# Optimization experiments

Hardware: AMD Instinct MI355X
Metric: run time of the kernel (lower is better)

Reference implementation:

```python
import jax, jax.numpy as jnp
import numpy as np

B, T, D, H, L, W = 32, 512, 256, 8, 2, 10
NQ = 10000
HD = D // H


def setup_inputs():
    key = jax.random.key(0)
    ks = jax.random.split(key, 16)
    def n(k, shape, s=0.02):
        return jax.random.normal(k, shape, jnp.float32) * s
    return {
        "q": jax.random.randint(ks[0], (B, T), 0, NQ),
        "s": jax.random.randint(ks[1], (B, T), 0, 2),
        "q_embed": n(ks[2], (NQ + 1, D)),
        "s_embed": n(ks[3], (2, D)),
        "pos_embed": n(ks[4], (512, D)),
        "fusion_w": n(ks[5], (2 * D, D)),
        "fusion_b": jnp.zeros((D,), jnp.float32),
        "in_proj_w": n(ks[6], (L, D, 3 * D)),
        "in_proj_b": jnp.zeros((L, 3 * D), jnp.float32),
        "out_proj_w": n(ks[7], (L, D, D)),
        "out_proj_b": jnp.zeros((L, D), jnp.float32),
        "ln1_g": jnp.ones((L, D), jnp.float32),
        "ln1_b": jnp.zeros((L, D), jnp.float32),
        "ln2_g": jnp.ones((L, D), jnp.float32),
        "ln2_b": jnp.zeros((L, D), jnp.float32),
        "ff1_w": n(ks[8], (L, D, 4 * D)),
        "ff1_b": jnp.zeros((L, 4 * D), jnp.float32),
        "ff2_w": n(ks[9], (L, 4 * D, D)),
        "ff2_b": jnp.zeros((L, D), jnp.float32),
        "sw1": n(ks[10], (6, 32), 0.1),
        "sb1": jnp.zeros((32,), jnp.float32),
        "sw2": n(ks[11], (32, D // 4), 0.1),
        "sb2": jnp.zeros((D // 4,), jnp.float32),
        "cw1": n(ks[12], (D + D // 4, D)),
        "cb1": jnp.zeros((D,), jnp.float32),
        "cw2": n(ks[13], (D, 1)),
        "cb2": jnp.zeros((1,), jnp.float32),
    }


def _ln(x, g, b):
    mu = jnp.mean(x, -1, keepdims=True)
    var = jnp.mean(jnp.square(x - mu), -1, keepdims=True)
    return (x - mu) * jax.lax.rsqrt(var + 1e-5) * g + b


def _sliding_sum(x, w):
    # sum over trailing window of size w ending at each t, via prefix sums
    c = jnp.concatenate([jnp.zeros((x.shape[0], 1), x.dtype), jnp.cumsum(x, axis=1)], axis=1)
    t = jnp.arange(x.shape[1])
    return c[:, t + 1] - c[:, jnp.maximum(t + 1 - w, 0)]


def _stats(s, mask):
    # vectorized version of _extract_statistics (prefix-sum sliding windows)
    mf = mask.astype(jnp.float32)
    sf = s.astype(jnp.float32) * mf
    valid = _sliding_sum(mf, W)
    correct_rate = _sliding_sum(sf, W) / (valid + 1e-6)
    rc = _sliding_sum(mf, 5)
    recent_correct = _sliding_sum(sf, 5) / (rc + 1e-6)
    trans = ((s[:, 1:] != s[:, :-1]) & mask[:, 1:] & mask[:, :-1]).astype(jnp.float32)
    diff = jnp.concatenate([jnp.zeros((s.shape[0], 1), jnp.float32), trans], axis=1)
    change_rate = _sliding_sum(diff, W - 1) / (valid + 1e-6)
    # max consecutive equal run within each trailing window of size W
    sp = jnp.pad(s, ((0, 0), (W - 1, 0)))
    mp = jnp.pad(mask, ((0, 0), (W - 1, 0)))
    win_s = [sp[:, j:j + T] for j in range(W)]
    win_m = [mp[:, j:j + T] for j in range(W)]
    run = win_m[0].astype(jnp.float32)
    mx = run
    for j in range(1, W):  # fixed small window, not a data-dim loop
        eq = (win_s[j] == win_s[j - 1]) & win_m[j - 1]
        run = win_m[j].astype(jnp.float32) * (jnp.where(eq, run, 0.0) + 1.0)
        mx = jnp.maximum(mx, run)
    rel = jnp.broadcast_to(jnp.arange(T, dtype=jnp.float32) / max(T, 100), s.shape)
    cov = valid / W
    return jnp.stack([correct_rate, recent_correct, change_rate, mx / W, rel, cov], axis=-1)


def reference(q, s, q_embed, s_embed, pos_embed, fusion_w, fusion_b, in_proj_w, in_proj_b,
              out_proj_w, out_proj_b, ln1_g, ln1_b, ln2_g, ln2_b, ff1_w, ff1_b, ff2_w, ff2_b,
              sw1, sb1, sw2, sb2, cw1, cb1, cw2, cb2):
    mask = s >= 0
    qm = jnp.where(mask, q, 0)
    sm = jnp.where(mask, s, 0)
    h = jnp.concatenate([q_embed[qm], s_embed[sm]], axis=-1)  # [B,T,2D]
    h = jax.nn.relu(h @ fusion_w + fusion_b) + pos_embed[:T][None]
    causal = jnp.tril(jnp.ones((T, T), bool))
    allowed = causal[None, None] & mask[:, None, None, :]
    scale = 1.0 / (HD ** 0.5)
    for l in range(L):
        qkv = h @ in_proj_w[l] + in_proj_b[l]
        qh, kh, vh = jnp.split(qkv, 3, axis=-1)
        qh = qh.reshape(B, T, H, HD).transpose(0, 2, 1, 3)
        kh = kh.reshape(B, T, H, HD).transpose(0, 2, 1, 3)
        vh = vh.reshape(B, T, H, HD).transpose(0, 2, 1, 3)
        scores = jnp.einsum('bhqd,bhkd->bhqk', qh, kh) * scale
        scores = jnp.where(allowed, scores, -1e9)
        attn = jax.nn.softmax(scores, axis=-1)
        o = jnp.einsum('bhqk,bhkd->bhqd', attn, vh).transpose(0, 2, 1, 3).reshape(B, T, D)
        h = _ln(h + (o @ out_proj_w[l] + out_proj_b[l]), ln1_g[l], ln1_b[l])
        ff = jax.nn.gelu(h @ ff1_w[l] + ff1_b[l], approximate=False) @ ff2_w[l] + ff2_b[l]
        h = _ln(h + ff, ln2_g[l], ln2_b[l])
    sfeat = _stats(sm, mask)  # [B,T,6]
    semb = jax.nn.relu(sfeat @ sw1 + sb1) @ sw2 + sb2  # [B,T,D//4]
    comb = jnp.concatenate([h, semb], axis=-1)
    logits = (jax.nn.relu(comb @ cw1 + cb1) @ cw2 + cb2)[..., 0]
    return jnp.where(mask, logits, -1e9)
```

## Files before the change

### kernel.cpp

```cpp
#include <hip/hip_runtime.h>
#include <hip/hip_bf16.h>
#include <cmath>


using short8 = __attribute__((ext_vector_type(8))) short;
using short4v = __attribute__((ext_vector_type(4))) short;
using f32x4  = __attribute__((ext_vector_type(4))) float;

__device__ inline float gelu_f(float x) {
    return 0.5f * x * (1.0f + erff(x * 0.70710678118654752f));
}

__device__ inline short f2bf(float x) {
    union { float f; unsigned u; } v; v.f = x;
    return (short)((v.u + 0x7fffu + ((v.u >> 16) & 1u)) >> 16);
}

__device__ inline float bf2f(short v) {
    union { unsigned u; float f; } x; x.u = ((unsigned)(unsigned short)v) << 16;
    return x.f;
}

__device__ inline unsigned packbf(float lo, float hi) {
    union { float f; unsigned u; } a, b; a.f = lo; b.f = hi;
    unsigned ra = (a.u + 0x7fffu + ((a.u >> 16) & 1u)) >> 16;
    unsigned rb = (b.u + 0x7fffu + ((b.u >> 16) & 1u)) >> 16;
    return (rb << 16) | (ra & 0xffffu);
}

#define GLOAD16(gp, lp) __builtin_amdgcn_global_load_lds( \
    (const __attribute__((address_space(1))) void*)(gp), \
    (__attribute__((address_space(3))) void*)(lp), 16, 0, 0)

__global__ __launch_bounds__(256) void prep(
    const float* __restrict__ fusion_w, const float* __restrict__ in_proj_w,
    const float* __restrict__ out_proj_w, const float* __restrict__ ff1_w,
    const float* __restrict__ ff2_w, const float* __restrict__ cw1,
    short* __restrict__ wts,
    const int* __restrict__ q, const int* __restrict__ s,
    const float* __restrict__ qe, const float* __restrict__ se,
    short* __restrict__ A,
    short* __restrict__ semb,
    const float* __restrict__ sw1, const float* __restrict__ sb1,
    const float* __restrict__ sw2, const float* __restrict__ sb2)
{
    __shared__ float tile[32][33];
    __shared__ float sv_sh[512];
    __shared__ float m_sh[512];
    __shared__ float sw2_sh[2048];

    if (blockIdx.x < 1744) {
        const int b0[10]      = {0,128,320,512,576,640,896,1152,1408,1664};
        const int Ks[10]      = {512,256,256,256,256,256,256,1024,1024,320};
        const int Ns[10]      = {256,768,768,256,256,1024,1024,256,256,256};
        const int sidx[10]    = {0,1,1,2,2,3,3,4,4,5};
        const size_t soff[10] = {0,0,196608,0,65536,0,262144,0,262144,0};
        const size_t doff[10] = {0,131072,327680,524288,589824,655360,917504,1179648,1441792,1703936};
        const float* srcs[6] = {fusion_w, in_proj_w, out_proj_w, ff1_w, ff2_w, cw1};
        int bid = blockIdx.x;
        int mi = 0;
        while (mi < 9 && bid >= b0[mi + 1]) ++mi;
        int bl = bid - b0[mi];
        int K = Ks[mi], N = Ns[mi];
        int tx = bl % (N >> 5), ty = bl / (N >> 5);
        const float* src = srcs[sidx[mi]] + soff[mi];
        short* dst = wts + doff[mi];
        int c = threadIdx.x & 31, r = threadIdx.x >> 5;
#pragma unroll
        for (int i = 0; i < 4; ++i)
            tile[r + i * 8][c] = src[(size_t)(ty * 32 + r + i * 8) * N + tx * 32 + c];
        __syncthreads();
#pragma unroll
        for (int i = 0; i < 4; ++i)
            dst[(size_t)(tx * 32 + r + i * 8) * K + ty * 32 + c] = f2bf(tile[c][r + i * 8]);
    } else if (blockIdx.x < 5840) {
        int e8 = (blockIdx.x - 1744) * 256 + threadIdx.x;
        int row = e8 >> 6;
        int k8 = (e8 & 63) << 3;
        int sv = s[row];
        bool mk = sv >= 0;
        const float* src = (k8 < 256) ? qe + (size_t)(mk ? q[row] : 0) * 256 + k8
                                      : se + (size_t)(mk ? sv : 0) * 256 + (k8 - 256);
        float4 v0 = *(const float4*)src;
        float4 v1 = *(const float4*)(src + 4);
        short8 o;
        o[0] = f2bf(v0.x); o[1] = f2bf(v0.y); o[2] = f2bf(v0.z); o[3] = f2bf(v0.w);
        o[4] = f2bf(v1.x); o[5] = f2bf(v1.y); o[6] = f2bf(v1.z); o[7] = f2bf(v1.w);
        *(short8*)(A + (size_t)row * 512 + k8) = o;
    } else {
        const int b = blockIdx.x - 5840;
        const int tt = threadIdx.x;
        for (int t = tt; t < 512; t += 256) {
            int sval = s[b * 512 + t];
            bool mk = sval >= 0;
            sv_sh[t] = mk ? (float)sval : 0.f;
            m_sh[t] = mk ? 1.f : 0.f;
        }
        for (int i = tt; i < 2048; i += 256) sw2_sh[i] = sw2[i];
        __syncthreads();
        for (int half = 0; half < 2; ++half) {
            const int t = tt + half * 256;
            float mf10 = 0, sf10 = 0, mf5 = 0, sf5 = 0, d9 = 0;
#pragma unroll
            for (int k = 0; k < 10; ++k) {
                int idx = t - k;
                if (idx >= 0) {
                    float mv = m_sh[idx], sv = sv_sh[idx];
                    mf10 += mv; sf10 += sv;
                    if (k < 5) { mf5 += mv; sf5 += sv; }
                    if (k < 9 && idx >= 1) {
                        if (sv != sv_sh[idx - 1] && mv > 0.5f && m_sh[idx - 1] > 0.5f) d9 += 1.f;
                    }
                }
            }
            float run, mx;
            {
                int x0 = t - 9;
                run = (x0 >= 0) ? m_sh[x0] : 0.f;
                mx = run;
#pragma unroll
                for (int j = 1; j < 10; ++j) {
                    int xc = t + j - 9, xp = xc - 1;
                    float sc = (xc >= 0) ? sv_sh[xc] : 0.f;
                    float sp = (xp >= 0) ? sv_sh[xp] : 0.f;
                    float mc = (xc >= 0) ? m_sh[xc] : 0.f;
                    float mp = (xp >= 0) ? m_sh[xp] : 0.f;
                    bool eq = (sc == sp) && (mp > 0.5f);
                    run = (mc > 0.5f) ? ((eq ? run : 0.f) + 1.f) : 0.f;
                    mx = fmaxf(mx, run);
                }
            }
            float f[6];
            f[0] = sf10 / (mf10 + 1e-6f);
            f[1] = sf5 / (mf5 + 1e-6f);
            f[2] = d9 / (mf10 + 1e-6f);
            f[3] = mx * 0.1f;
            f[4] = (float)t * (1.f / 512.f);
            f[5] = mf10 * 0.1f;

            float hid[32];
#pragma unroll
            for (int j2 = 0; j2 < 32; ++j2) {
                float a = sb1[j2];
#pragma unroll
                for (int i = 0; i < 6; ++i) a = fmaf(f[i], sw1[i * 32 + j2], a);
                hid[j2] = fmaxf(a, 0.f);
            }
            short* orow = semb + ((size_t)b * 512 + t) * 64;
            for (int c = 0; c < 64; c += 4) {
                float v0 = sb2[c], v1 = sb2[c + 1], v2 = sb2[c + 2], v3 = sb2[c + 3];
#pragma unroll
                for (int j2 = 0; j2 < 32; ++j2) {
                    float hh = hid[j2];
                    v0 = fmaf(hh, sw2_sh[j2 * 64 + c], v0);
                    v1 = fmaf(hh, sw2_sh[j2 * 64 + c + 1], v1);
                    v2 = fmaf(hh, sw2_sh[j2 * 64 + c + 2], v2);
                    v3 = fmaf(hh, sw2_sh[j2 * 64 + c + 3], v3);
                }
                short4v o; o[0] = f2bf(v0); o[1] = f2bf(v1); o[2] = f2bf(v2); o[3] = f2bf(v3);
                *(short4v*)(orow + c) = o;
            }
        }
    }
}

template<int EPI, int KTOT>
__global__ __launch_bounds__(512) void kbs(
    const short* __restrict__ A, const short* __restrict__ A2,
    const short* __restrict__ Wt, const float* __restrict__ bias,
    short* __restrict__ o0, short* __restrict__ o1, short* __restrict__ o2,
    float* __restrict__ xb, short* __restrict__ hb,
    const float* __restrict__ pos, const float* __restrict__ cw2v,
    float* __restrict__ pbuf)
{
    constexpr int BN = 64;
    constexpr int NCH = (KTOT + 255) / 256;
    constexpr int KA = (EPI == 4) ? 256 : KTOT;
    __shared__ short Bs[BN * 256];
    const int tid = threadIdx.x, lane = tid & 63, wv = tid >> 6;
    const int lg = lane >> 4, lr = lane & 15;
    const int n0 = blockIdx.y * BN;
    const int row0 = blockIdx.x * 128 + wv * 16;

    f32x4 acc[4] = {};
    short8 af[8];

#pragma unroll
    for (int c = 0; c < NCH; ++c) {
        const int ck = (KTOT - c * 256 >= 256) ? 256 : (KTOT - c * 256);
        const int spr = ck >> 3;
        if (c) __syncthreads();
        for (int i = 0; i < (BN * ck) / 8; i += 512) {
            int slot = i + tid;
            int n = slot / spr, posn = slot % spr;
            int g = posn ^ (n & 7);
            GLOAD16(Wt + (size_t)(n0 + n) * KTOT + c * 256 + g * 8, &Bs[slot * 8]);
        }
        const int nkk = ck >> 5;
        if (EPI == 4 && c == 1) {
            const short* ar2 = A2 + (size_t)(row0 + lr) * 64 + lg * 8;
            af[0] = *(const short8*)(ar2);
            af[1] = *(const short8*)(ar2 + 32);
        } else {
            const short* ar = A + (size_t)(row0 + lr) * KA + c * 256 + lg * 8;
#pragma unroll
            for (int kk = 0; kk < 8; ++kk)
                if (kk < nkk) af[kk] = *(const short8*)(ar + kk * 32);
        }
        __syncthreads();
#pragma unroll
        for (int kk = 0; kk < 8; ++kk) {
            if (kk >= nkk) break;
#pragma unroll
            for (int j = 0; j < 4; ++j) {
                int n = j * 16 + lr;
                short8 b = *(const short8*)&Bs[n * ck + (((kk * 4 + lg) ^ (n & 7)) << 3)];
                acc[j] = __builtin_amdgcn_mfma_f32_16x16x32_bf16(af[kk], b, acc[j], 0, 0, 0);
            }
        }
    }

    if constexpr (EPI == 0) {
#pragma unroll
        for (int j = 0; j < 4; ++j)
#pragma unroll
        for (int r = 0; r < 4; ++r) {
            int row = row0 + lg * 4 + r;
            int col = n0 + j * 16 + lr;
            float x = acc[j][r] + bias[col];
            x = fmaxf(x, 0.f) + pos[(size_t)(row & 511) * 256 + col];
            o0[(size_t)row * 256 + col] = f2bf(x);
        }
    } else if constexpr (EPI == 1) {
#pragma unroll
        for (int j = 0; j < 4; ++j)
#pragma unroll
        for (int r = 0; r < 4; ++r) {
            int row = row0 + lg * 4 + r;
            int gcol = n0 + j * 16 + lr;
            int t = row & 511, bg = row >> 9;
            int sec = gcol >> 8, cc = gcol & 255;
            int h = cc >> 5, d = cc & 31, bh = bg * 8 + h;
            short v = f2bf(acc[j][r] + bias[gcol]);
            if (sec == 0)      o0[((size_t)bh * 512 + t) * 32 + d] = v;
            else if (sec == 1) o1[((size_t)bh * 512 + t) * 32 + d] = v;
            else {
                int kl = t & 31;
                o2[(size_t)bh * 16384 + (size_t)(t >> 5) * 1024 +
                   (size_t)((kl >> 2) & 3) * 256 + d * 8 + (((kl & 3) << 1) | ((kl >> 4) & 1))] = v;
            }
        }
    } else if constexpr (EPI == 2) {
#pragma unroll
        for (int j = 0; j < 4; ++j)
#pragma unroll
        for (int r = 0; r < 4; ++r) {
            int row = row0 + lg * 4 + r;
            int gcol = n0 + j * 16 + lr;
            float x = acc[j][r] + bias[gcol];
            o0[(size_t)row * 1024 + gcol] = f2bf(gelu_f(x));
        }
    } else if constexpr (EPI == 3) {
#pragma unroll
        for (int j = 0; j < 4; ++j)
#pragma unroll
        for (int r = 0; r < 4; ++r) {
            int row = row0 + lg * 4 + r;
            int col = n0 + j * 16 + lr;
            xb[(size_t)row * 256 + col] =
                acc[j][r] + bias[col] + bf2f(hb[(size_t)row * 256 + col]);
        }
    } else {
#pragma unroll
        for (int r = 0; r < 4; ++r) {
            float p = 0.f;
#pragma unroll
            for (int j = 0; j < 4; ++j) {
                int col = n0 + j * 16 + lr;
                float v = fmaxf(acc[j][r] + bias[col], 0.f);
                p += v * cw2v[col];
            }
#pragma unroll
            for (int off = 1; off < 16; off <<= 1) p += __shfl_xor(p, off);
            if (lr == 0) {
                int row = row0 + lg * 4 + r;
                pbuf[(size_t)blockIdx.y * 16384 + row] = p;
            }
        }
    }
}

__global__ __launch_bounds__(256) void k_ln(
    const float* __restrict__ xb, short* __restrict__ hb,
    const float* __restrict__ gamma, const float* __restrict__ beta)
{
    int row = blockIdx.x * 4 + (threadIdx.x >> 6);
    int lane = threadIdx.x & 63;
    int c = lane * 4;
    float4 xv = *reinterpret_cast<const float4*>(xb + (size_t)row * 256 + c);
    float sm = xv.x + xv.y + xv.z + xv.w;
    float sq = xv.x * xv.x + xv.y * xv.y + xv.z * xv.z + xv.w * xv.w;
#pragma unroll
    for (int off = 32; off > 0; off >>= 1) {
        sm += __shfl_xor(sm, off);
        sq += __shfl_xor(sq, off);
    }
    float mu = sm * (1.f / 256.f);
    float var = sq * (1.f / 256.f) - mu * mu;
    float rstd = rsqrtf(var + 1e-5f);
    float4 gv = *reinterpret_cast<const float4*>(gamma + c);
    float4 bv = *reinterpret_cast<const float4*>(beta + c);
    short4v o;
    o[0] = f2bf((xv.x - mu) * rstd * gv.x + bv.x);
    o[1] = f2bf((xv.y - mu) * rstd * gv.y + bv.y);
    o[2] = f2bf((xv.z - mu) * rstd * gv.z + bv.z);
    o[3] = f2bf((xv.w - mu) * rstd * gv.w + bv.w);
    *(short4v*)(hb + (size_t)row * 256 + c) = o;
}

__global__ __launch_bounds__(256) void k_fin(
    const float* __restrict__ pbuf, const int* __restrict__ s,
    const float* __restrict__ cb2, float* __restrict__ out)
{
    int i = blockIdx.x * 256 + threadIdx.x;
    float v = pbuf[i] + pbuf[i + 16384] + pbuf[i + 32768] + pbuf[i + 49152] + cb2[0];
    out[i] = (s[i] >= 0) ? v : -1e9f;
}

__global__ __launch_bounds__(256) void attn_mfma(
    const short* __restrict__ Qg, const short* __restrict__ Kg,
    const short* __restrict__ VTg, short* __restrict__ O)
{
    __shared__ unsigned Wp[4][16][20];
    const int bh = blockIdx.x >> 2, part = blockIdx.x & 3;
    const int b = bh >> 3, h = bh & 7;
    const int wv = threadIdx.x >> 6, lane = threadIdx.x & 63;
    const int lg = lane >> 4, lr = lane & 15;
    const int slot = part * 4 + wv;
    const short* Qbh = Qg + (size_t)bh * 16384;
    const short* Kbh = Kg + (size_t)bh * 16384;
    const short* Vbh = VTg + (size_t)bh * 16384;
    const float scale = 0.17677669529663687f;

    for (int half = 0; half < 2; ++half) {
        const int tile = half ? (31 - slot) : slot;
        const int q0 = tile << 4;
        short8 qa = *(const short8*)(Qbh + (size_t)(q0 + lr) * 32 + lg * 8);
        f32x4 o0 = {}, o1 = {};
        float l_[4] = {0.f, 0.f, 0.f, 0.f};
        const int nfull = q0 >> 5;

        for (int c = 0; c <= nfull; ++c) {
            int kc = c << 5;
            short8 kf0 = *(const short8*)(Kbh + (size_t)(kc + lr) * 32 + lg * 8);
            short8 kf1 = *(const short8*)(Kbh + (size_t)(kc + 16 + lr) * 32 + lg * 8);
            f32x4 s0 = {}, s1 = {};
            s0 = __builtin_amdgcn_mfma_f32_16x16x32_bf16(qa, kf0, s0, 0, 0, 0);
            s1 = __builtin_amdgcn_mfma_f32_16x16x32_bf16(qa, kf1, s1, 0, 0, 0);
            float p0[4], p1[4];
            if (c < nfull) {
#pragma unroll
                for (int r = 0; r < 4; ++r) {
                    p0[r] = __expf(s0[r] * scale);
                    p1[r] = __expf(s1[r] * scale);
                }
            } else {
#pragma unroll
                for (int r = 0; r < 4; ++r) {
                    int qq = q0 + lg * 4 + r;
                    p0[r] = (kc + lr)      > qq ? 0.f : __expf(s0[r] * scale);
                    p1[r] = (kc + 16 + lr) > qq ? 0.f : __expf(s1[r] * scale);
                }
            }
#pragma unroll
            for (int r = 0; r < 4; ++r) {
                l_[r] += p0[r] + p1[r];
                Wp[wv][lg * 4 + r][lr] = packbf(p0[r], p1[r]);
            }
            short8 pa = *(const short8*)&Wp[wv][lr][lg * 4];
            short8 vf0 = *(const short8*)(Vbh + (size_t)c * 1024 + lg * 256 + lr * 8);
            short8 vf1 = *(const short8*)(Vbh + (size_t)c * 1024 + lg * 256 + (lr + 16) * 8);
            o0 = __builtin_amdgcn_mfma_f32_16x16x32_bf16(pa, vf0, o0, 0, 0, 0);
            o1 = __builtin_amdgcn_mfma_f32_16x16x32_bf16(pa, vf1, o1, 0, 0, 0);
        }
#pragma unroll
        for (int off = 1; off < 16; off <<= 1)
#pragma unroll
            for (int r = 0; r < 4; ++r) l_[r] += __shfl_xor(l_[r], off);
#pragma unroll
        for (int r = 0; r < 4; ++r) {
            float inv = 1.f / l_[r];
            size_t ro = ((size_t)b * 512 + q0 + lg * 4 + r) * 256 + h * 32;
            O[ro + lr] = f2bf(o0[r] * inv);
            O[ro + 16 + lr] = f2bf(o1[r] * inv);
        }
    }
}

extern "C" void kernel_launch(void* const* d_in, const int* in_sizes, int n_in,
                              void* d_out, int out_size, void* d_ws, size_t ws_size,
                              hipStream_t stream) {
    const int*   q         = (const int*)d_in[0];
    const int*   s         = (const int*)d_in[1];
    const float* q_embed   = (const float*)d_in[2];
    const float* s_embed   = (const float*)d_in[3];
    const float* pos_embed = (const float*)d_in[4];
    const float* fusion_w  = (const float*)d_in[5];
    const float* fusion_b  = (const float*)d_in[6];
    const float* in_proj_w = (const float*)d_in[7];
    const float* in_proj_b = (const float*)d_in[8];
    const float* out_proj_w= (const float*)d_in[9];
    const float* out_proj_b= (const float*)d_in[10];
    const float* ln1_g     = (const float*)d_in[11];
    const float* ln1_b     = (const float*)d_in[12];
    const float* ln2_g     = (const float*)d_in[13];
    const float* ln2_b     = (const float*)d_in[14];
    const float* ff1_w     = (const float*)d_in[15];
    const float* ff1_b     = (const float*)d_in[16];
    const float* ff2_w     = (const float*)d_in[17];
    const float* ff2_b     = (const float*)d_in[18];
    const float* sw1       = (const float*)d_in[19];
    const float* sb1       = (const float*)d_in[20];
    const float* sw2       = (const float*)d_in[21];
    const float* sb2       = (const float*)d_in[22];
    const float* cw1       = (const float*)d_in[23];
    const float* cb1       = (const float*)d_in[24];
    const float* cw2       = (const float*)d_in[25];
    const float* cb2       = (const float*)d_in[26];
    float* out = (float*)d_out;

    char* base = (char*)d_ws;
    short* hb   = (short*)(base);
    short* bufA = (short*)(base + 8388608);
    short* att  = (short*)(base + 41943040);
    short* Qg   = (short*)(base + 50331648);
    short* Kg   = (short*)(base + 58720256);
    short* VTg  = (short*)(base + 67108864);
    short* semb = (short*)(base + 75497472);
    short* wts  = (short*)(base + 77594624);
    float* xb   = (float*)(base + 81166336);
    float* pbuf = (float*)(base + 97943552);

    const size_t W_FUSION = 0, W_INPROJ0 = 131072, W_INPROJ1 = 327680;
    const size_t W_OUTPROJ0 = 524288, W_OUTPROJ1 = 589824;
    const size_t W_FF1_0 = 655360, W_FF1_1 = 917504;
    const size_t W_FF2_0 = 1179648, W_FF2_1 = 1441792;
    const size_t W_CW1 = 1703936;

    prep<<<5872, 256, 0, stream>>>(fusion_w, in_proj_w, out_proj_w,
                                   ff1_w, ff2_w, cw1, wts,
                                   q, s, q_embed, s_embed, bufA,
                                   semb, sw1, sb1, sw2, sb2);
    kbs<0, 512><<<dim3(128, 4), 512, 0, stream>>>(bufA, nullptr,
        wts + W_FUSION, fusion_b, hb, nullptr, nullptr, nullptr, nullptr,
        pos_embed, nullptr, nullptr);
    for (int l = 0; l < 2; ++l) {
        kbs<1, 256><<<dim3(128, 12), 512, 0, stream>>>(hb, nullptr,
            wts + (l ? W_INPROJ1 : W_INPROJ0), in_proj_b + l * 768,
            Qg, Kg, VTg, nullptr, nullptr, nullptr, nullptr, nullptr);
        attn_mfma<<<1024, 256, 0, stream>>>(Qg, Kg, VTg, att);
        kbs<3, 256><<<dim3(128, 4), 512, 0, stream>>>(att, nullptr,
            wts + (l ? W_OUTPROJ1 : W_OUTPROJ0), out_proj_b + l * 256,
            nullptr, nullptr, nullptr, xb, hb, nullptr, nullptr, nullptr);
        k_ln<<<4096, 256, 0, stream>>>(xb, hb, ln1_g + l * 256, ln1_b + l * 256);
        kbs<2, 256><<<dim3(128, 16), 512, 0, stream>>>(hb, nullptr,
            wts + (l ? W_FF1_1 : W_FF1_0), ff1_b + l * 1024,
            bufA, nullptr, nullptr, nullptr, nullptr, nullptr, nullptr, nullptr);
        kbs<3, 1024><<<dim3(128, 4), 512, 0, stream>>>(bufA, nullptr,
            wts + (l ? W_FF2_1 : W_FF2_0), ff2_b + l * 256,
            nullptr, nullptr, nullptr, xb, hb, nullptr, nullptr, nullptr);
        k_ln<<<4096, 256, 0, stream>>>(xb, hb, ln2_g + l * 256, ln2_b + l * 256);
    }
    kbs<4, 320><<<dim3(128, 4), 512, 0, stream>>>(hb, semb,
        wts + W_CW1, cb1, nullptr, nullptr, nullptr, nullptr, nullptr,
        nullptr, cw2, pbuf);
    k_fin<<<64, 256, 0, stream>>>(pbuf, s, cb2, out);
}
```

Measured before the change: 289.8 us.

## Fuse embedding gather into fusion GEMM, store residual as bf16, interleave attention tiles

```diff
diff --git a/kernel.cpp b/kernel.cpp
--- a/kernel.cpp
+++ b/kernel.cpp
@@ -37,9 +37,7 @@
     const float* __restrict__ out_proj_w, const float* __restrict__ ff1_w,
     const float* __restrict__ ff2_w, const float* __restrict__ cw1,
     short* __restrict__ wts,
-    const int* __restrict__ q, const int* __restrict__ s,
-    const float* __restrict__ qe, const float* __restrict__ se,
-    short* __restrict__ A,
+    const int* __restrict__ s,
     short* __restrict__ semb,
     const float* __restrict__ sw1, const float* __restrict__ sb1,
     const float* __restrict__ sw2, const float* __restrict__ sb2)
@@ -73,22 +71,8 @@
 #pragma unroll
         for (int i = 0; i < 4; ++i)
             dst[(size_t)(tx * 32 + r + i * 8) * K + ty * 32 + c] = f2bf(tile[c][r + i * 8]);
-    } else if (blockIdx.x < 5840) {
-        int e8 = (blockIdx.x - 1744) * 256 + threadIdx.x;
-        int row = e8 >> 6;
-        int k8 = (e8 & 63) << 3;
-        int sv = s[row];
-        bool mk = sv >= 0;
-        const float* src = (k8 < 256) ? qe + (size_t)(mk ? q[row] : 0) * 256 + k8
-                                      : se + (size_t)(mk ? sv : 0) * 256 + (k8 - 256);
-        float4 v0 = *(const float4*)src;
-        float4 v1 = *(const float4*)(src + 4);
-        short8 o;
-        o[0] = f2bf(v0.x); o[1] = f2bf(v0.y); o[2] = f2bf(v0.z); o[3] = f2bf(v0.w);
-        o[4] = f2bf(v1.x); o[5] = f2bf(v1.y); o[6] = f2bf(v1.z); o[7] = f2bf(v1.w);
-        *(short8*)(A + (size_t)row * 512 + k8) = o;
     } else {
-        const int b = blockIdx.x - 5840;
+        const int b = blockIdx.x - 1744;
         const int tt = threadIdx.x;
         for (int t = tt; t < 512; t += 256) {
             int sval = s[b * 512 + t];
@@ -169,9 +153,11 @@
     const short* __restrict__ A, const short* __restrict__ A2,
     const short* __restrict__ Wt, const float* __restrict__ bias,
     short* __restrict__ o0, short* __restrict__ o1, short* __restrict__ o2,
-    float* __restrict__ xb, short* __restrict__ hb,
+    short* __restrict__ xbb, short* __restrict__ hb,
     const float* __restrict__ pos, const float* __restrict__ cw2v,
-    float* __restrict__ pbuf)
+    float* __restrict__ pbuf,
+    const int* __restrict__ qi, const int* __restrict__ si,
+    const float* __restrict__ qe, const float* __restrict__ se)
 {
     constexpr int BN = 64;
     constexpr int NCH = (KTOT + 255) / 256;
@@ -197,7 +183,23 @@
             GLOAD16(Wt + (size_t)(n0 + n) * KTOT + c * 256 + g * 8, &Bs[slot * 8]);
         }
         const int nkk = ck >> 5;
-        if (EPI == 4 && c == 1) {
+        if constexpr (EPI == 0) {
+            int row = row0 + lr;
+            int sv = si[row];
+            bool mk = sv >= 0;
+            const float* base = (c == 0) ? qe + (size_t)(mk ? qi[row] : 0) * 256
+                                         : se + (size_t)(mk ? sv : 0) * 256;
+#pragma unroll
+            for (int kk = 0; kk < 8; ++kk) {
+                const float* p = base + kk * 32 + lg * 8;
+                float4 v0 = *(const float4*)p;
+                float4 v1 = *(const float4*)(p + 4);
+                short8 o;
+                o[0] = f2bf(v0.x); o[1] = f2bf(v0.y); o[2] = f2bf(v0.z); o[3] = f2bf(v0.w);
+                o[4] = f2bf(v1.x); o[5] = f2bf(v1.y); o[6] = f2bf(v1.z); o[7] = f2bf(v1.w);
+                af[kk] = o;
+            }
+        } else if (EPI == 4 && c == 1) {
             const short* ar2 = A2 + (size_t)(row0 + lr) * 64 + lg * 8;
             af[0] = *(const short8*)(ar2);
             af[1] = *(const short8*)(ar2 + 32);
@@ -267,8 +269,8 @@
         for (int r = 0; r < 4; ++r) {
             int row = row0 + lg * 4 + r;
             int col = n0 + j * 16 + lr;
-            xb[(size_t)row * 256 + col] =
-                acc[j][r] + bias[col] + bf2f(hb[(size_t)row * 256 + col]);
+            xbb[(size_t)row * 256 + col] =
+                f2bf(acc[j][r] + bias[col] + bf2f(hb[(size_t)row * 256 + col]));
         }
     } else {
 #pragma unroll
@@ -291,15 +293,16 @@
 }
 
 __global__ __launch_bounds__(256) void k_ln(
-    const float* __restrict__ xb, short* __restrict__ hb,
+    const short* __restrict__ xbb, short* __restrict__ hb,
     const float* __restrict__ gamma, const float* __restrict__ beta)
 {
     int row = blockIdx.x * 4 + (threadIdx.x >> 6);
     int lane = threadIdx.x & 63;
     int c = lane * 4;
-    float4 xv = *reinterpret_cast<const float4*>(xb + (size_t)row * 256 + c);
-    float sm = xv.x + xv.y + xv.z + xv.w;
-    float sq = xv.x * xv.x + xv.y * xv.y + xv.z * xv.z + xv.w * xv.w;
+    short4v xv4 = *(const short4v*)(xbb + (size_t)row * 256 + c);
+    float x0 = bf2f(xv4[0]), x1 = bf2f(xv4[1]), x2 = bf2f(xv4[2]), x3 = bf2f(xv4[3]);
+    float sm = x0 + x1 + x2 + x3;
+    float sq = x0 * x0 + x1 * x1 + x2 * x2 + x3 * x3;
 #pragma unroll
     for (int off = 32; off > 0; off >>= 1) {
         sm += __shfl_xor(sm, off);
@@ -311,10 +314,10 @@
     float4 gv = *reinterpret_cast<const float4*>(gamma + c);
     float4 bv = *reinterpret_cast<const float4*>(beta + c);
     short4v o;
-    o[0] = f2bf((xv.x - mu) * rstd * gv.x + bv.x);
-    o[1] = f2bf((xv.y - mu) * rstd * gv.y + bv.y);
-    o[2] = f2bf((xv.z - mu) * rstd * gv.z + bv.z);
-    o[3] = f2bf((xv.w - mu) * rstd * gv.w + bv.w);
+    o[0] = f2bf((x0 - mu) * rstd * gv.x + bv.x);
+    o[1] = f2bf((x1 - mu) * rstd * gv.y + bv.y);
+    o[2] = f2bf((x2 - mu) * rstd * gv.z + bv.z);
+    o[3] = f2bf((x3 - mu) * rstd * gv.w + bv.w);
     *(short4v*)(hb + (size_t)row * 256 + c) = o;
 }
 
@@ -331,7 +334,7 @@
     const short* __restrict__ Qg, const short* __restrict__ Kg,
     const short* __restrict__ VTg, short* __restrict__ O)
 {
-    __shared__ unsigned Wp[4][16][20];
+    __shared__ unsigned Wp[4][2][16][20];
     const int bh = blockIdx.x >> 2, part = blockIdx.x & 3;
     const int b = bh >> 3, h = bh & 7;
     const int wv = threadIdx.x >> 6, lane = threadIdx.x & 63;
@@ -342,58 +345,84 @@
     const short* Vbh = VTg + (size_t)bh * 16384;
     const float scale = 0.17677669529663687f;
 
-    for (int half = 0; half < 2; ++half) {
-        const int tile = half ? (31 - slot) : slot;
-        const int q0 = tile << 4;
-        short8 qa = *(const short8*)(Qbh + (size_t)(q0 + lr) * 32 + lg * 8);
-        f32x4 o0 = {}, o1 = {};
-        float l_[4] = {0.f, 0.f, 0.f, 0.f};
-        const int nfull = q0 >> 5;
-
-        for (int c = 0; c <= nfull; ++c) {
-            int kc = c << 5;
-            short8 kf0 = *(const short8*)(Kbh + (size_t)(kc + lr) * 32 + lg * 8);
-            short8 kf1 = *(const short8*)(Kbh + (size_t)(kc + 16 + lr) * 32 + lg * 8);
-            f32x4 s0 = {}, s1 = {};
-            s0 = __builtin_amdgcn_mfma_f32_16x16x32_bf16(qa, kf0, s0, 0, 0, 0);
-            s1 = __builtin_amdgcn_mfma_f32_16x16x32_bf16(qa, kf1, s1, 0, 0, 0);
-            float p0[4], p1[4];
-            if (c < nfull) {
-#pragma unroll
-                for (int r = 0; r < 4; ++r) {
-                    p0[r] = __expf(s0[r] * scale);
-                    p1[r] = __expf(s1[r] * scale);
-                }
-            } else {
-#pragma unroll
-                for (int r = 0; r < 4; ++r) {
-                    int qq = q0 + lg * 4 + r;
-                    p0[r] = (kc + lr)      > qq ? 0.f : __expf(s0[r] * scale);
-                    p1[r] = (kc + 16 + lr) > qq ? 0.f : __expf(s1[r] * scale);
-                }
-            }
+    const int tA = slot, tB = 31 - slot;
+    const int qA0 = tA << 4, qB0 = tB << 4;
+    const int nA = tA >> 1, nB = tB >> 1;
+    short8 qaA = *(const short8*)(Qbh + (size_t)(qA0 + lr) * 32 + lg * 8);
+    short8 qaB = *(const short8*)(Qbh + (size_t)(qB0 + lr) * 32 + lg * 8);
+    f32x4 oA0 = {}, oA1 = {}, oB0 = {}, oB1 = {};
+    float lA[4] = {0.f, 0.f, 0.f, 0.f};
+    float lB[4] = {0.f, 0.f, 0.f, 0.f};
+
+    auto chunk = [&](int c, int q0, int nfull, const short8& qa,
+                     const short8& kf0, const short8& kf1,
+                     const short8& vf0, const short8& vf1,
+                     f32x4& o0, f32x4& o1, float* l_, int slab) {
+        int kc = c << 5;
+        f32x4 s0 = {}, s1 = {};
+        s0 = __builtin_amdgcn_mfma_f32_16x16x32_bf16(qa, kf0, s0, 0, 0, 0);
+        s1 = __builtin_amdgcn_mfma_f32_16x16x32_bf16(qa, kf1, s1, 0, 0, 0);
+        float p0[4], p1[4];
+        if (c < nfull) {
 #pragma unroll
             for (int r = 0; r < 4; ++r) {
-                l_[r] += p0[r] + p1[r];
-                Wp[wv][lg * 4 + r][lr] = packbf(p0[r], p1[r]);
-            }
-            short8 pa = *(const short8*)&Wp[wv][lr][lg * 4];
-            short8 vf0 = *(const short8*)(Vbh + (size_t)c * 1024 + lg * 256 + lr * 8);
-            short8 vf1 = *(const short8*)(Vbh + (size_t)c * 1024 + lg * 256 + (lr + 16) * 8);
-            o0 = __builtin_amdgcn_mfma_f32_16x16x32_bf16(pa, vf0, o0, 0, 0, 0);
-            o1 = __builtin_amdgcn_mfma_f32_16x16x32_bf16(pa, vf1, o1, 0, 0, 0);
-        }
-#pragma unroll
-        for (int off = 1; off < 16; off <<= 1)
-#pragma unroll
-            for (int r = 0; r < 4; ++r) l_[r] += __shfl_xor(l_[r], off);
-#pragma unroll
-        for (int r = 0; r < 4; ++r) {
-            float inv = 1.f / l_[r];
-            size_t ro = ((size_t)b * 512 + q0 + lg * 4 + r) * 256 + h * 32;
-            O[ro + lr] = f2bf(o0[r] * inv);
-            O[ro + 16 + lr] = f2bf(o1[r] * inv);
-        }
+                p0[r] = __expf(s0[r] * scale);
+                p1[r] = __expf(s1[r] * scale);
+            }
+        } else {
+#pragma unroll
+            for (int r = 0; r < 4; ++r) {
+                int qq = q0 + lg * 4 + r;
+                p0[r] = (kc + lr)      > qq ? 0.f : __expf(s0[r] * scale);
+                p1[r] = (kc + 16 + lr) > qq ? 0.f : __expf(s1[r] * scale);
+            }
+        }
+#pragma unroll
+        for (int r = 0; r < 4; ++r) {
+            l_[r] += p0[r] + p1[r];
+            Wp[wv][slab][lg * 4 + r][lr] = packbf(p0[r], p1[r]);
+        }
+        short8 pa = *(const short8*)&Wp[wv][slab][lr][lg * 4];
+        o0 = __builtin_amdgcn_mfma_f32_16x16x32_bf16(pa, vf0, o0, 0, 0, 0);
+        o1 = __builtin_amdgcn_mfma_f32_16x16x32_bf16(pa, vf1, o1, 0, 0, 0);
+    };
+
+    int c = 0;
+    for (; c <= nA; ++c) {
+        int kc = c << 5;
+        short8 kf0 = *(const short8*)(Kbh + (size_t)(kc + lr) * 32 + lg * 8);
+        short8 kf1 = *(const short8*)(Kbh + (size_t)(kc + 16 + lr) * 32 + lg * 8);
+        short8 vf0 = *(const short8*)(Vbh + (size_t)c * 1024 + lg * 256 + lr * 8);
+        short8 vf1 = *(const short8*)(Vbh + (size_t)c * 1024 + lg * 256 + (lr + 16) * 8);
+        chunk(c, qB0, nB, qaB, kf0, kf1, vf0, vf1, oB0, oB1, lB, 1);
+        chunk(c, qA0, nA, qaA, kf0, kf1, vf0, vf1, oA0, oA1, lA, 0);
+    }
+    for (; c <= nB; ++c) {
+        int kc = c << 5;
+        short8 kf0 = *(const short8*)(Kbh + (size_t)(kc + lr) * 32 + lg * 8);
+        short8 kf1 = *(const short8*)(Kbh + (size_t)(kc + 16 + lr) * 32 + lg * 8);
+        short8 vf0 = *(const short8*)(Vbh + (size_t)c * 1024 + lg * 256 + lr * 8);
+        short8 vf1 = *(const short8*)(Vbh + (size_t)c * 1024 + lg * 256 + (lr + 16) * 8);
+        chunk(c, qB0, nB, qaB, kf0, kf1, vf0, vf1, oB0, oB1, lB, 1);
+    }
+
+#pragma unroll
+    for (int off = 1; off < 16; off <<= 1)
+#pragma unroll
+        for (int r = 0; r < 4; ++r) {
+            lA[r] += __shfl_xor(lA[r], off);
+            lB[r] += __shfl_xor(lB[r], off);
+        }
+#pragma unroll
+    for (int r = 0; r < 4; ++r) {
+        float invA = 1.f / lA[r];
+        size_t roA = ((size_t)b * 512 + qA0 + lg * 4 + r) * 256 + h * 32;
+        O[roA + lr] = f2bf(oA0[r] * invA);
+        O[roA + 16 + lr] = f2bf(oA1[r] * invA);
+        float invB = 1.f / lB[r];
+        size_t roB = ((size_t)b * 512 + qB0 + lg * 4 + r) * 256 + h * 32;
+        O[roB + lr] = f2bf(oB0[r] * invB);
+        O[roB + 16 + lr] = f2bf(oB1[r] * invB);
     }
 }
 
@@ -438,8 +467,8 @@
     short* VTg  = (short*)(base + 67108864);
     short* semb = (short*)(base + 75497472);
     short* wts  = (short*)(base + 77594624);
-    float* xb   = (float*)(base + 81166336);
-    float* pbuf = (float*)(base + 97943552);
+    short* xbb  = (short*)(base + 81166336);
+    float* pbuf = (float*)(base + 89554944);
 
     const size_t W_FUSION = 0, W_INPROJ0 = 131072, W_INPROJ1 = 327680;
     const size_t W_OUTPROJ0 = 524288, W_OUTPROJ1 = 589824;
@@ -447,32 +476,35 @@
     const size_t W_FF2_0 = 1179648, W_FF2_1 = 1441792;
     const size_t W_CW1 = 1703936;
 
-    prep<<<5872, 256, 0, stream>>>(fusion_w, in_proj_w, out_proj_w,
+    prep<<<1776, 256, 0, stream>>>(fusion_w, in_proj_w, out_proj_w,
                                    ff1_w, ff2_w, cw1, wts,
-                                   q, s, q_embed, s_embed, bufA,
-                                   semb, sw1, sb1, sw2, sb2);
-    kbs<0, 512><<<dim3(128, 4), 512, 0, stream>>>(bufA, nullptr,
+                                   s, semb, sw1, sb1, sw2, sb2);
+    kbs<0, 512><<<dim3(128, 4), 512, 0, stream>>>(nullptr, nullptr,
         wts + W_FUSION, fusion_b, hb, nullptr, nullptr, nullptr, nullptr,
-        pos_embed, nullptr, nullptr);
+        pos_embed, nullptr, nullptr, q, s, q_embed, s_embed);
     for (int l = 0; l < 2; ++l) {
         kbs<1, 256><<<dim3(128, 12), 512, 0, stream>>>(hb, nullptr,
             wts + (l ? W_INPROJ1 : W_INPROJ0), in_proj_b + l * 768,
-            Qg, Kg, VTg, nullptr, nullptr, nullptr, nullptr, nullptr);
+            Qg, Kg, VTg, nullptr, nullptr, nullptr, nullptr, nullptr,
+            nullptr, nullptr, nullptr, nullptr);
         attn_mfma<<<1024, 256, 0, stream>>>(Qg, Kg, VTg, att);
         kbs<3, 256><<<dim3(128, 4), 512, 0, stream>>>(att, nullptr,
             wts + (l ? W_OUTPROJ1 : W_OUTPROJ0), out_proj_b + l * 256,
-            nullptr, nullptr, nullptr, xb, hb, nullptr, nullptr, nullptr);
-        k_ln<<<4096, 256, 0, stream>>>(xb, hb, ln1_g + l * 256, ln1_b + l * 256);
+            nullptr, nullptr, nullptr, xbb, hb, nullptr, nullptr, nullptr,
+            nullptr, nullptr, nullptr, nullptr);
+        k_ln<<<4096, 256, 0, stream>>>(xbb, hb, ln1_g + l * 256, ln1_b + l * 256);
         kbs<2, 256><<<dim3(128, 16), 512, 0, stream>>>(hb, nullptr,
             wts + (l ? W_FF1_1 : W_FF1_0), ff1_b + l * 1024,
-            bufA, nullptr, nullptr, nullptr, nullptr, nullptr, nullptr, nullptr);
+            bufA, nullptr, nullptr, nullptr, nullptr, nullptr, nullptr, nullptr,
+            nullptr, nullptr, nullptr, nullptr);
         kbs<3, 1024><<<dim3(128, 4), 512, 0, stream>>>(bufA, nullptr,
             wts + (l ? W_FF2_1 : W_FF2_0), ff2_b + l * 256,
-            nullptr, nullptr, nullptr, xb, hb, nullptr, nullptr, nullptr);
-        k_ln<<<4096, 256, 0, stream>>>(xb, hb, ln2_g + l * 256, ln2_b + l * 256);
+            nullptr, nullptr, nullptr, xbb, hb, nullptr, nullptr, nullptr,
+            nullptr, nullptr, nullptr, nullptr);
+        k_ln<<<4096, 256, 0, stream>>>(xbb, hb, ln2_g + l * 256, ln2_b + l * 256);
     }
     kbs<4, 320><<<dim3(128, 4), 512, 0, stream>>>(hb, semb,
         wts + W_CW1, cb1, nullptr, nullptr, nullptr, nullptr, nullptr,
-        nullptr, cw2, pbuf);
+        nullptr, cw2, pbuf, nullptr, nullptr, nullptr, nullptr);
     k_fin<<<64, 256, 0, stream>>>(pbuf, s, cb2, out);
 }
```

Measured after the change: 285.0 us. No clear change (-1.7%).
